# Kernel optimization log

Measured on AMD Instinct MI355X. Metric: run time of the kernel, lower is better.

The kernel has to match this reference:

```python
import jax, jax.numpy as jnp
import numpy as np

B, N, C, F, E, K = 4, 4096, 1024, 4096, 8, 2

def setup_inputs() -> dict:
    key = jax.random.key(0)
    ks = jax.random.split(key, 6)
    x = jax.random.normal(ks[0], (B, N, C), dtype=jnp.float32)
    router_w = jax.random.normal(ks[1], (E, C), dtype=jnp.float32) * 0.02  # nn.Linear weight [out,in]
    w1 = jax.random.normal(ks[2], (E, C, F), dtype=jnp.float32) * (1.0 / np.sqrt(C))
    b1 = jnp.zeros((E, F), dtype=jnp.float32)
    w2 = jax.random.normal(ks[3], (E, F, C), dtype=jnp.float32) * (1.0 / np.sqrt(F))
    b2 = jnp.zeros((E, C), dtype=jnp.float32)
    return {"x": x, "router_w": router_w, "w1": w1, "b1": b1, "w2": w2, "b2": b2}

def reference(x, router_w, w1, b1, w2, b2):
    Bx, Nx, Cx = x.shape
    xf = x.reshape(-1, Cx)                                  # [T, C]
    logits = xf @ router_w.T                                # [T, E]
    probs = jax.nn.softmax(logits, axis=-1)
    top_w, top_i = jax.lax.top_k(probs, K)                  # [T, K]
    top_w = top_w / (jnp.sum(top_w, axis=-1, keepdims=True) + 1e-9)
    out = jnp.zeros_like(xf)
    for e in range(E):
        # combine weight for expert e per token (0 if not routed)
        gate = jnp.sum(jnp.where(top_i == e, top_w, 0.0), axis=-1)   # [T]
        h = jax.nn.gelu(xf @ w1[e] + b1[e], approximate=False)       # [T, F]
        y = h @ w2[e] + b2[e]                                        # [T, C]
        out = out + gate[:, None] * y
    return out.reshape(Bx, Nx, Cx)
```

## Files before the change

### kernel.cpp

```cpp
#include <hip/hip_runtime.h>
#include <hip/hip_fp16.h>

#define T_TOK 16384
#define C_DIM 1024
#define F_DIM 4096
#define E_NUM 8

typedef _Float16 half8 __attribute__((ext_vector_type(8)));
typedef _Float16 half4v __attribute__((ext_vector_type(4)));
typedef float f32x4 __attribute__((ext_vector_type(4)));

static constexpr size_t META_OFF  = 0;
static constexpr size_t XB_OFF    = 256;
static constexpr size_t W1T_OFF   = XB_OFF  + (size_t)2*T_TOK*C_DIM;
static constexpr size_t W2T_OFF   = W1T_OFF + (size_t)2*E_NUM*C_DIM*F_DIM;
static constexpr size_t HB_OFF    = W2T_OFF + (size_t)2*E_NUM*C_DIM*F_DIM;
static constexpr size_t YB_OFF    = HB_OFF  + (size_t)2*T_TOK*2*F_DIM;
static constexpr size_t TOK_OFF   = YB_OFF  + (size_t)2*T_TOK*2*C_DIM;
static constexpr size_t GATE_OFF  = TOK_OFF + (size_t)4*E_NUM*T_TOK;
static constexpr size_t TSLOT_OFF = GATE_OFF+ (size_t)4*E_NUM*T_TOK;
static constexpr size_t EPAIR_OFF = TSLOT_OFF + (size_t)4*T_TOK*2;
static constexpr size_t GPAIR_OFF = EPAIR_OFF + (size_t)4*T_TOK;
static constexpr size_t WS_NEED   = GPAIR_OFF + (size_t)8*T_TOK;

__device__ __forceinline__ void async16(void* lds, const void* g) {
  __builtin_amdgcn_global_load_lds((const __attribute__((address_space(1))) unsigned int*)g,
                                   (__attribute__((address_space(3))) unsigned int*)lds,
                                   16, 0, 0);
}

__global__ __launch_bounds__(256) void transpose_cast_kernel(const float* __restrict__ in,
                                                             _Float16* __restrict__ outp,
                                                             int R, int Cc) {
  __shared__ float tile[64][65];
  int e = blockIdx.z;
  const float* ip = in + (size_t)e * R * Cc;
  _Float16* op = outp + (size_t)e * R * Cc;
  int c0 = blockIdx.x * 64, r0 = blockIdx.y * 64;
  int tid = threadIdx.x;
  int lr = tid >> 4, lc = (tid & 15) * 4;
  #pragma unroll
  for (int d = 0; d < 4; ++d) {
    int row = lr + d * 16;
    float4 v = *(const float4*)(ip + (size_t)(r0 + row) * Cc + c0 + lc);
    tile[row][lc]     = v.x;
    tile[row][lc + 1] = v.y;
    tile[row][lc + 2] = v.z;
    tile[row][lc + 3] = v.w;
  }
  __syncthreads();
  int oc = tid >> 3, or8 = (tid & 7) * 8;
  #pragma unroll
  for (int d = 0; d < 2; ++d) {
    int c = oc + d * 32;
    half8 h;
    #pragma unroll
    for (int j = 0; j < 8; ++j) h[j] = (_Float16)tile[or8 + j][c];
    *(half8*)(op + (size_t)(c0 + c) * R + r0 + or8) = h;
  }
}

__global__ __launch_bounds__(256) void router_kernel(const float* __restrict__ x,
                                                     const float* __restrict__ rw,
                                                     int* __restrict__ epair,
                                                     float2* __restrict__ gpair,
                                                     _Float16* __restrict__ xb) {
  int wv = threadIdx.x >> 6, l = threadIdx.x & 63;
  int t = blockIdx.x * 4 + wv;
  const float* xr = x + (size_t)t * C_DIM;
  double acc[E_NUM] = {};
  #pragma unroll
  for (int j = 0; j < 4; ++j) {
    float4 xv = *(const float4*)(xr + j * 256 + l * 4);
    half4v hv;
    hv[0] = (_Float16)xv.x; hv[1] = (_Float16)xv.y;
    hv[2] = (_Float16)xv.z; hv[3] = (_Float16)xv.w;
    *(half4v*)(xb + (size_t)t * C_DIM + j * 256 + l * 4) = hv;
    #pragma unroll
    for (int e = 0; e < E_NUM; ++e) {
      float4 w4 = *(const float4*)(rw + (size_t)e * C_DIM + j * 256 + l * 4);
      acc[e] += (double)xv.x * w4.x + (double)xv.y * w4.y +
                (double)xv.z * w4.z + (double)xv.w * w4.w;
    }
  }
  #pragma unroll
  for (int e = 0; e < E_NUM; ++e)
    #pragma unroll
    for (int off = 32; off; off >>= 1)
      acc[e] += __shfl_xor(acc[e], off, 64);

  if (l == 0) {
    double m = acc[0];
    #pragma unroll
    for (int e = 1; e < E_NUM; ++e) m = acc[e] > m ? acc[e] : m;
    double p[E_NUM], s = 0.0;
    #pragma unroll
    for (int e = 0; e < E_NUM; ++e) { p[e] = exp(acc[e] - m); s += p[e]; }
    int i0 = 0; double b0 = p[0];
    #pragma unroll
    for (int e = 1; e < E_NUM; ++e) if (p[e] > b0) { b0 = p[e]; i0 = e; }
    int i1 = -1; double b1v = -1.0;
    #pragma unroll
    for (int e = 0; e < E_NUM; ++e) if (e != i0 && p[e] > b1v) { b1v = p[e]; i1 = e; }
    double q0 = b0 / s, q1 = b1v / s;
    double den = q0 + q1 + 1e-9;
    epair[t] = i0 | (i1 << 8);
    gpair[t] = make_float2((float)(q0 / den), (float)(q1 / den));
  }
}

__global__ __launch_bounds__(1024) void assign_kernel(const int* __restrict__ epair,
                                                      const float2* __restrict__ gpair,
                                                      int* __restrict__ counts,
                                                      int* __restrict__ tok,
                                                      float* __restrict__ gate,
                                                      int* __restrict__ tslot) {
  __shared__ int wsum[16];
  __shared__ int wbase[16];
  __shared__ int stot;
  int myE = blockIdx.x;
  int tid = threadIdx.x, wid = tid >> 6, lane = tid & 63;
  int base = 0;
  for (int it = 0; it < (T_TOK * 2) / 1024; ++it) {
    int idx = it * 1024 + tid;
    int t = idx >> 1, k = idx & 1;
    int ep = epair[t];
    int e = (k ? (ep >> 8) : ep) & 0xff;
    bool f = (e == myE);
    unsigned long long mask = __ballot(f);
    int lanep = __popcll(mask & ((1ull << lane) - 1ull));
    if (lane == 0) wsum[wid] = __popcll(mask);
    __syncthreads();
    if (tid == 0) {
      int s = 0;
      #pragma unroll
      for (int i = 0; i < 16; ++i) { wbase[i] = s; s += wsum[i]; }
      stot = s;
    }
    __syncthreads();
    if (f) {
      int slot = base + wbase[wid] + lanep;
      float2 g = gpair[t];
      tok[myE * T_TOK + slot] = t;
      gate[myE * T_TOK + slot] = k ? g.y : g.x;
      tslot[idx] = (myE << 24) | slot;
    }
    base += stot;
  }
  if (tid == 0) counts[myE] = base;
}

__global__ void plan_kernel(int* meta) {
  if (threadIdx.x == 0 && blockIdx.x == 0) {
    int ro = 0, to = 0;
    meta[8] = 0; meta[17] = 0;
    for (int e = 0; e < E_NUM; ++e) {
      int c = meta[e];
      ro += c; to += (c + 127) >> 7;
      meta[9 + e] = ro; meta[18 + e] = to;
    }
  }
}


__global__ __launch_bounds__(512) void gemm1_kernel(const _Float16* __restrict__ xb,
                                                    const _Float16* __restrict__ w1t,
                                                    const float* __restrict__ b1,
                                                    _Float16* __restrict__ hbuf,
                                                    const int* __restrict__ tok,
                                                    const int* __restrict__ meta) {
  __shared__ _Float16 smem[24576];
  __shared__ int tokLds[128];

  int bid = blockIdx.x;
  int swz = (bid & 7) * 528 + (bid >> 3);
  int band = swz >> 7, rem = swz & 127;
  int nt = rem >> 3;
  int mt = band * 8 + (rem & 7);
  if (mt >= meta[17 + E_NUM]) return;
  int e = 0;
  while (mt >= meta[18 + e]) ++e;
  int ne = meta[e];
  int r0 = (mt - meta[17 + e]) << 7;
  int valid = ne - r0; if (valid > 128) valid = 128;

  int tid = threadIdx.x;
  if (tid < 128) {
    int r = tid < valid ? tid : valid - 1;
    tokLds[tid] = tok[e * T_TOK + r0 + r];
  }
  __syncthreads();

  int row = tid >> 2, c4 = tid & 3;
  int ch = c4 ^ ((row >> 1) & 3);
  const _Float16* aSrc  = xb + (size_t)tokLds[row] * C_DIM + ch * 8;
  const _Float16* bSrc0 = w1t + ((size_t)e * F_DIM + nt * 256 + row) * C_DIM + ch * 8;
  const _Float16* bSrc1 = bSrc0 + (size_t)128 * C_DIM;

  char* SM = (char*)smem;
  char* dst = SM + (size_t)tid * 16;

  int w = tid >> 6, l = tid & 63;
  int wm = w >> 2, wn = w & 3;
  int rl = l & 15, q = l >> 4;
  int swq = (q ^ ((rl >> 1) & 3)) * 16;
  int aBy = wm * 4096 + rl * 64 + swq;
  int bBy = 16384 + wn * 4096 + rl * 64 + swq;

  f32x4 acc[4][4] = {};
  constexpr int NT = C_DIM / 64;
  for (int kt = 0; kt < NT; ++kt) {
    __syncthreads();
    int ko = kt * 64;
    async16(dst,          aSrc  + ko);
    async16(dst + 8192,   aSrc  + ko + 32);
    async16(dst + 16384,  bSrc0 + ko);
    async16(dst + 24576,  bSrc1 + ko);
    async16(dst + 32768,  bSrc0 + ko + 32);
    async16(dst + 40960,  bSrc1 + ko + 32);
    __syncthreads();
    #pragma unroll
    for (int ks = 0; ks < 2; ++ks) {
      half8 af[4], bf[4];
      #pragma unroll
      for (int m = 0; m < 4; ++m)
        af[m] = *(const half8*)(SM + ks * 8192 + aBy + m * 1024);
      #pragma unroll
      for (int n = 0; n < 4; ++n)
        bf[n] = *(const half8*)(SM + ks * 16384 + bBy + n * 1024);
      #pragma unroll
      for (int m = 0; m < 4; ++m)
        #pragma unroll
        for (int n = 0; n < 4; ++n)
          acc[m][n] = __builtin_amdgcn_mfma_f32_16x16x32_f16(af[m], bf[n], acc[m][n], 0, 0, 0);
    }
  }

  int hbase = meta[8 + e] + r0;
  float bv[4];
  #pragma unroll
  for (int n = 0; n < 4; ++n)
    bv[n] = b1[(size_t)e * F_DIM + nt * 256 + wn * 64 + n * 16 + rl];
  #pragma unroll
  for (int m = 0; m < 4; ++m) {
    int rb = wm * 64 + m * 16 + q * 4;
    #pragma unroll
    for (int n = 0; n < 4; ++n) {
      int col = nt * 256 + wn * 64 + n * 16 + rl;
      #pragma unroll
      for (int r = 0; r < 4; ++r) {
        int rr = rb + r;
        if (rr < valid) {
          float pre = acc[m][n][r] + bv[n];
          float g = 0.5f * pre * (1.0f + erff(pre * 0.70710678118654752f));
          hbuf[(size_t)(hbase + rr) * F_DIM + col] = (_Float16)g;
        }
      }
    }
  }
}

__global__ __launch_bounds__(256) void gemm2_kernel(const _Float16* __restrict__ hbuf,
                                                    const _Float16* __restrict__ w2t,
                                                    const float* __restrict__ b2,
                                                    _Float16* __restrict__ ybuf,
                                                    const float* __restrict__ gate,
                                                    const int* __restrict__ meta) {
  __shared__ _Float16 smem[16384];
  __shared__ float gateLds[128];

  int bid = blockIdx.x;
  int swz = (bid & 7) * 264 + (bid >> 3);
  int band = swz >> 6, rem = swz & 63;
  int nt = rem >> 3;
  int mt = band * 8 + (rem & 7);
  if (mt >= meta[17 + E_NUM]) return;
  int e = 0;
  while (mt >= meta[18 + e]) ++e;
  int ne = meta[e];
  int r0 = (mt - meta[17 + e]) << 7;
  int valid = ne - r0; if (valid > 128) valid = 128;
  int hbase = meta[8 + e] + r0;

  int tid = threadIdx.x;
  if (tid < 128) {
    int r = tid < valid ? tid : valid - 1;
    gateLds[tid] = gate[e * T_TOK + r0 + r];
  }
  __syncthreads();

  int row = tid >> 2, c4 = tid & 3;
  int ch = c4 ^ ((row >> 1) & 3);
  int rcA0 = row      < valid ? row      : valid - 1;
  int rcA1 = row + 64 < valid ? row + 64 : valid - 1;
  const _Float16* aSrc0 = hbuf + (size_t)(hbase + rcA0) * F_DIM + ch * 8;
  const _Float16* aSrc1 = hbuf + (size_t)(hbase + rcA1) * F_DIM + ch * 8;
  const _Float16* bSrc0 = w2t + ((size_t)e * C_DIM + nt * 128 + row) * F_DIM + ch * 8;
  const _Float16* bSrc1 = bSrc0 + (size_t)64 * F_DIM;

  char* SM = (char*)smem;
  char* dst = SM + (size_t)tid * 16;

  int w = tid >> 6, l = tid & 63;
  int wm = w >> 1, wn = w & 1;
  int rl = l & 15, q = l >> 4;
  int swq = (q ^ ((rl >> 1) & 3)) * 16;
  int aBy = wm * 4096 + rl * 64 + swq;
  int bBy = 16384 + wn * 4096 + rl * 64 + swq;

  f32x4 acc[4][4] = {};
  constexpr int NT = F_DIM / 64;
  for (int kt = 0; kt < NT; ++kt) {
    __syncthreads();
    int ko = kt * 64;
    async16(dst,          aSrc0 + ko);
    async16(dst + 4096,   aSrc1 + ko);
    async16(dst + 8192,   aSrc0 + ko + 32);
    async16(dst + 12288,  aSrc1 + ko + 32);
    async16(dst + 16384,  bSrc0 + ko);
    async16(dst + 20480,  bSrc1 + ko);
    async16(dst + 24576,  bSrc0 + ko + 32);
    async16(dst + 28672,  bSrc1 + ko + 32);
    __syncthreads();
    #pragma unroll
    for (int ks = 0; ks < 2; ++ks) {
      half8 af[4], bf[4];
      #pragma unroll
      for (int m = 0; m < 4; ++m)
        af[m] = *(const half8*)(SM + ks * 8192 + aBy + m * 1024);
      #pragma unroll
      for (int n = 0; n < 4; ++n)
        bf[n] = *(const half8*)(SM + ks * 8192 + bBy + n * 1024);
      #pragma unroll
      for (int m = 0; m < 4; ++m)
        #pragma unroll
        for (int n = 0; n < 4; ++n)
          acc[m][n] = __builtin_amdgcn_mfma_f32_16x16x32_f16(af[m], bf[n], acc[m][n], 0, 0, 0);
    }
  }

  float bv[4];
  #pragma unroll
  for (int n = 0; n < 4; ++n)
    bv[n] = b2[(size_t)e * C_DIM + nt * 128 + wn * 64 + n * 16 + rl];
  #pragma unroll
  for (int m = 0; m < 4; ++m) {
    int rb = wm * 64 + m * 16 + q * 4;
    #pragma unroll
    for (int n = 0; n < 4; ++n) {
      int col = nt * 128 + wn * 64 + n * 16 + rl;
      #pragma unroll
      for (int r = 0; r < 4; ++r) {
        int rr = rb + r;
        if (rr < valid) {
          float val = gateLds[rr] * (acc[m][n][r] + bv[n]);
          ybuf[(size_t)(hbase + rr) * C_DIM + col] = (_Float16)val;
        }
      }
    }
  }
}

__global__ __launch_bounds__(256) void combine_kernel(const _Float16* __restrict__ ybuf,
                                                      const int* __restrict__ tslot,
                                                      const int* __restrict__ meta,
                                                      float* __restrict__ out) {
  int gid = blockIdx.x * 256 + threadIdx.x;
  int t = gid >> 7;
  int cc = (gid & 127) << 3;
  int s0 = tslot[t * 2], s1 = tslot[t * 2 + 1];
  size_t r0 = (size_t)meta[8 + (s0 >> 24)] + (s0 & 0xFFFFFF);
  size_t r1 = (size_t)meta[8 + (s1 >> 24)] + (s1 & 0xFFFFFF);
  half8 y0 = *(const half8*)(ybuf + r0 * C_DIM + cc);
  half8 y1 = *(const half8*)(ybuf + r1 * C_DIM + cc);
  float4 o0, o1;
  o0.x = (float)y0[0] + (float)y1[0];
  o0.y = (float)y0[1] + (float)y1[1];
  o0.z = (float)y0[2] + (float)y1[2];
  o0.w = (float)y0[3] + (float)y1[3];
  o1.x = (float)y0[4] + (float)y1[4];
  o1.y = (float)y0[5] + (float)y1[5];
  o1.z = (float)y0[6] + (float)y1[6];
  o1.w = (float)y0[7] + (float)y1[7];
  *(float4*)(out + (size_t)t * C_DIM + cc) = o0;
  *(float4*)(out + (size_t)t * C_DIM + cc + 4) = o1;
}

extern "C" void kernel_launch(void* const* d_in, const int* in_sizes, int n_in,
                              void* d_out, int out_size, void* d_ws, size_t ws_size,
                              hipStream_t stream) {
  (void)in_sizes; (void)n_in; (void)out_size;
  if (!d_ws || ws_size < WS_NEED) return;

  const float* x  = (const float*)d_in[0];
  const float* rw = (const float*)d_in[1];
  const float* w1 = (const float*)d_in[2];
  const float* b1 = (const float*)d_in[3];
  const float* w2 = (const float*)d_in[4];
  const float* b2 = (const float*)d_in[5];
  float* out = (float*)d_out;

  char* ws = (char*)d_ws;
  int*       meta  = (int*)(ws + META_OFF);
  _Float16*  xb    = (_Float16*)(ws + XB_OFF);
  _Float16*  w1t   = (_Float16*)(ws + W1T_OFF);
  _Float16*  w2t   = (_Float16*)(ws + W2T_OFF);
  _Float16*  hbuf  = (_Float16*)(ws + HB_OFF);
  _Float16*  ybuf  = (_Float16*)(ws + YB_OFF);
  int*       tok   = (int*)(ws + TOK_OFF);
  float*     gate  = (float*)(ws + GATE_OFF);
  int*       tslot = (int*)(ws + TSLOT_OFF);
  int*       epair = (int*)(ws + EPAIR_OFF);
  float2*    gpair = (float2*)(ws + GPAIR_OFF);

  hipMemsetAsync(meta, 0, 256, stream);

  transpose_cast_kernel<<<dim3(F_DIM / 64, C_DIM / 64, E_NUM), 256, 0, stream>>>(w1, w1t, C_DIM, F_DIM);
  transpose_cast_kernel<<<dim3(C_DIM / 64, F_DIM / 64, E_NUM), 256, 0, stream>>>(w2, w2t, F_DIM, C_DIM);
  router_kernel<<<T_TOK / 4, 256, 0, stream>>>(x, rw, epair, gpair, xb);
  assign_kernel<<<E_NUM, 1024, 0, stream>>>(epair, gpair, meta, tok, gate, tslot);
  plan_kernel<<<1, 64, 0, stream>>>(meta);

  gemm1_kernel<<<264 * 16, 512, 0, stream>>>(xb, w1t, b1, hbuf, tok, meta);
  gemm2_kernel<<<264 * 8, 256, 0, stream>>>(hbuf, w2t, b2, ybuf, gate, meta);
  combine_kernel<<<(T_TOK * (C_DIM / 8)) / 256, 256, 0, stream>>>(ybuf, tslot, meta, out);
}
```

Measured before the change: 1.008 ms.

## Make expert GEMMs persistent with grid-stride tile loop and smaller gemm1 tiles

Both expert GEMM kernels become persistent: a fixed grid of 1024 blocks loops over the swizzled work tiles and skips empty ones, instead of launching one block per possible tile and exiting early. gemm1 also shrinks from 512-thread 128x256 tiles to 256-thread 128x128 tiles, matching gemm2. The intent is to cut the cost of launching and retiring many empty blocks and to improve load balance and occupancy. The trade-off is extra per-tile synchronisation, and the smaller gemm1 tile loads the A operand more times per output.

```diff
diff --git a/kernel.cpp b/kernel.cpp
--- a/kernel.cpp
+++ b/kernel.cpp
@@ -163,97 +163,106 @@
 }
 
 
-__global__ __launch_bounds__(512) void gemm1_kernel(const _Float16* __restrict__ xb,
+#define GEMM_GRID 1024
+
+__global__ __launch_bounds__(256) void gemm1_kernel(const _Float16* __restrict__ xb,
                                                     const _Float16* __restrict__ w1t,
                                                     const float* __restrict__ b1,
                                                     _Float16* __restrict__ hbuf,
                                                     const int* __restrict__ tok,
                                                     const int* __restrict__ meta) {
-  __shared__ _Float16 smem[24576];
+  __shared__ _Float16 smem[16384];
   __shared__ int tokLds[128];
 
-  int bid = blockIdx.x;
-  int swz = (bid & 7) * 528 + (bid >> 3);
-  int band = swz >> 7, rem = swz & 127;
-  int nt = rem >> 3;
-  int mt = band * 8 + (rem & 7);
-  if (mt >= meta[17 + E_NUM]) return;
-  int e = 0;
-  while (mt >= meta[18 + e]) ++e;
-  int ne = meta[e];
-  int r0 = (mt - meta[17 + e]) << 7;
-  int valid = ne - r0; if (valid > 128) valid = 128;
-
   int tid = threadIdx.x;
-  if (tid < 128) {
-    int r = tid < valid ? tid : valid - 1;
-    tokLds[tid] = tok[e * T_TOK + r0 + r];
-  }
-  __syncthreads();
-
   int row = tid >> 2, c4 = tid & 3;
   int ch = c4 ^ ((row >> 1) & 3);
-  const _Float16* aSrc  = xb + (size_t)tokLds[row] * C_DIM + ch * 8;
-  const _Float16* bSrc0 = w1t + ((size_t)e * F_DIM + nt * 256 + row) * C_DIM + ch * 8;
-  const _Float16* bSrc1 = bSrc0 + (size_t)128 * C_DIM;
-
-  char* SM = (char*)smem;
-  char* dst = SM + (size_t)tid * 16;
-
-  int w = tid >> 6, l = tid & 63;
-  int wm = w >> 2, wn = w & 3;
+  int w0 = tid >> 6, l = tid & 63;
+  int wm = w0 >> 1, wn = w0 & 1;
   int rl = l & 15, q = l >> 4;
   int swq = (q ^ ((rl >> 1) & 3)) * 16;
   int aBy = wm * 4096 + rl * 64 + swq;
   int bBy = 16384 + wn * 4096 + rl * 64 + swq;
-
-  f32x4 acc[4][4] = {};
-  constexpr int NT = C_DIM / 64;
-  for (int kt = 0; kt < NT; ++kt) {
-    __syncthreads();
-    int ko = kt * 64;
-    async16(dst,          aSrc  + ko);
-    async16(dst + 8192,   aSrc  + ko + 32);
-    async16(dst + 16384,  bSrc0 + ko);
-    async16(dst + 24576,  bSrc1 + ko);
-    async16(dst + 32768,  bSrc0 + ko + 32);
-    async16(dst + 40960,  bSrc1 + ko + 32);
-    __syncthreads();
-    #pragma unroll
-    for (int ks = 0; ks < 2; ++ks) {
-      half8 af[4], bf[4];
+  char* SM = (char*)smem;
+  char* dst = SM + (size_t)tid * 16;
+
+  constexpr int NWORK = 264 * 32;
+  int nTiles = meta[17 + E_NUM];
+
+  for (int wk = blockIdx.x; wk < NWORK; wk += GEMM_GRID) {
+    int swz = (wk & 7) * (NWORK / 8) + (wk >> 3);
+    int band = swz >> 8, rem = swz & 255;
+    int nt = rem >> 3;
+    int mt = band * 8 + (rem & 7);
+    if (mt >= nTiles) continue;
+    int e = 0;
+    while (mt >= meta[18 + e]) ++e;
+    int ne = meta[e];
+    int r0 = (mt - meta[17 + e]) << 7;
+    int valid = ne - r0; if (valid > 128) valid = 128;
+
+    __syncthreads();
+    if (tid < 128) {
+      int r = tid < valid ? tid : valid - 1;
+      tokLds[tid] = tok[e * T_TOK + r0 + r];
+    }
+    __syncthreads();
+
+    const _Float16* aSrc0 = xb + (size_t)tokLds[row] * C_DIM + ch * 8;
+    const _Float16* aSrc1 = xb + (size_t)tokLds[row + 64] * C_DIM + ch * 8;
+    const _Float16* bSrc0 = w1t + ((size_t)e * F_DIM + nt * 128 + row) * C_DIM + ch * 8;
+    const _Float16* bSrc1 = bSrc0 + (size_t)64 * C_DIM;
+
+    f32x4 acc[4][4] = {};
+    constexpr int NT = C_DIM / 64;
+    for (int kt = 0; kt < NT; ++kt) {
+      __syncthreads();
+      int ko = kt * 64;
+      async16(dst,          aSrc0 + ko);
+      async16(dst + 4096,   aSrc1 + ko);
+      async16(dst + 8192,   aSrc0 + ko + 32);
+      async16(dst + 12288,  aSrc1 + ko + 32);
+      async16(dst + 16384,  bSrc0 + ko);
+      async16(dst + 20480,  bSrc1 + ko);
+      async16(dst + 24576,  bSrc0 + ko + 32);
+      async16(dst + 28672,  bSrc1 + ko + 32);
+      __syncthreads();
       #pragma unroll
-      for (int m = 0; m < 4; ++m)
-        af[m] = *(const half8*)(SM + ks * 8192 + aBy + m * 1024);
+      for (int ks = 0; ks < 2; ++ks) {
+        half8 af[4], bf[4];
+        #pragma unroll
+        for (int m = 0; m < 4; ++m)
+          af[m] = *(const half8*)(SM + ks * 8192 + aBy + m * 1024);
+        #pragma unroll
+        for (int n = 0; n < 4; ++n)
+          bf[n] = *(const half8*)(SM + ks * 8192 + bBy + n * 1024);
+        #pragma unroll
+        for (int m = 0; m < 4; ++m)
+          #pragma unroll
+          for (int n = 0; n < 4; ++n)
+            acc[m][n] = __builtin_amdgcn_mfma_f32_16x16x32_f16(af[m], bf[n], acc[m][n], 0, 0, 0);
+      }
+    }
+
+    int hbase = meta[8 + e] + r0;
+    float bv[4];
+    #pragma unroll
+    for (int n = 0; n < 4; ++n)
+      bv[n] = b1[(size_t)e * F_DIM + nt * 128 + wn * 64 + n * 16 + rl];
+    #pragma unroll
+    for (int m = 0; m < 4; ++m) {
+      int rb = wm * 64 + m * 16 + q * 4;
       #pragma unroll
-      for (int n = 0; n < 4; ++n)
-        bf[n] = *(const half8*)(SM + ks * 16384 + bBy + n * 1024);
-      #pragma unroll
-      for (int m = 0; m < 4; ++m)
-        #pragma unroll
-        for (int n = 0; n < 4; ++n)
-          acc[m][n] = __builtin_amdgcn_mfma_f32_16x16x32_f16(af[m], bf[n], acc[m][n], 0, 0, 0);
-    }
-  }
-
-  int hbase = meta[8 + e] + r0;
-  float bv[4];
-  #pragma unroll
-  for (int n = 0; n < 4; ++n)
-    bv[n] = b1[(size_t)e * F_DIM + nt * 256 + wn * 64 + n * 16 + rl];
-  #pragma unroll
-  for (int m = 0; m < 4; ++m) {
-    int rb = wm * 64 + m * 16 + q * 4;
-    #pragma unroll
-    for (int n = 0; n < 4; ++n) {
-      int col = nt * 256 + wn * 64 + n * 16 + rl;
-      #pragma unroll
-      for (int r = 0; r < 4; ++r) {
-        int rr = rb + r;
-        if (rr < valid) {
-          float pre = acc[m][n][r] + bv[n];
-          float g = 0.5f * pre * (1.0f + erff(pre * 0.70710678118654752f));
-          hbuf[(size_t)(hbase + rr) * F_DIM + col] = (_Float16)g;
+      for (int n = 0; n < 4; ++n) {
+        int col = nt * 128 + wn * 64 + n * 16 + rl;
+        #pragma unroll
+        for (int r = 0; r < 4; ++r) {
+          int rr = rb + r;
+          if (rr < valid) {
+            float pre = acc[m][n][r] + bv[n];
+            float g = 0.5f * pre * (1.0f + erff(pre * 0.70710678118654752f));
+            hbuf[(size_t)(hbase + rr) * F_DIM + col] = (_Float16)g;
+          }
         }
       }
     }
@@ -269,92 +278,96 @@
   __shared__ _Float16 smem[16384];
   __shared__ float gateLds[128];
 
-  int bid = blockIdx.x;
-  int swz = (bid & 7) * 264 + (bid >> 3);
-  int band = swz >> 6, rem = swz & 63;
-  int nt = rem >> 3;
-  int mt = band * 8 + (rem & 7);
-  if (mt >= meta[17 + E_NUM]) return;
-  int e = 0;
-  while (mt >= meta[18 + e]) ++e;
-  int ne = meta[e];
-  int r0 = (mt - meta[17 + e]) << 7;
-  int valid = ne - r0; if (valid > 128) valid = 128;
-  int hbase = meta[8 + e] + r0;
-
   int tid = threadIdx.x;
-  if (tid < 128) {
-    int r = tid < valid ? tid : valid - 1;
-    gateLds[tid] = gate[e * T_TOK + r0 + r];
-  }
-  __syncthreads();
-
   int row = tid >> 2, c4 = tid & 3;
   int ch = c4 ^ ((row >> 1) & 3);
-  int rcA0 = row      < valid ? row      : valid - 1;
-  int rcA1 = row + 64 < valid ? row + 64 : valid - 1;
-  const _Float16* aSrc0 = hbuf + (size_t)(hbase + rcA0) * F_DIM + ch * 8;
-  const _Float16* aSrc1 = hbuf + (size_t)(hbase + rcA1) * F_DIM + ch * 8;
-  const _Float16* bSrc0 = w2t + ((size_t)e * C_DIM + nt * 128 + row) * F_DIM + ch * 8;
-  const _Float16* bSrc1 = bSrc0 + (size_t)64 * F_DIM;
-
-  char* SM = (char*)smem;
-  char* dst = SM + (size_t)tid * 16;
-
-  int w = tid >> 6, l = tid & 63;
-  int wm = w >> 1, wn = w & 1;
+  int w0 = tid >> 6, l = tid & 63;
+  int wm = w0 >> 1, wn = w0 & 1;
   int rl = l & 15, q = l >> 4;
   int swq = (q ^ ((rl >> 1) & 3)) * 16;
   int aBy = wm * 4096 + rl * 64 + swq;
   int bBy = 16384 + wn * 4096 + rl * 64 + swq;
-
-  f32x4 acc[4][4] = {};
-  constexpr int NT = F_DIM / 64;
-  for (int kt = 0; kt < NT; ++kt) {
-    __syncthreads();
-    int ko = kt * 64;
-    async16(dst,          aSrc0 + ko);
-    async16(dst + 4096,   aSrc1 + ko);
-    async16(dst + 8192,   aSrc0 + ko + 32);
-    async16(dst + 12288,  aSrc1 + ko + 32);
-    async16(dst + 16384,  bSrc0 + ko);
-    async16(dst + 20480,  bSrc1 + ko);
-    async16(dst + 24576,  bSrc0 + ko + 32);
-    async16(dst + 28672,  bSrc1 + ko + 32);
-    __syncthreads();
-    #pragma unroll
-    for (int ks = 0; ks < 2; ++ks) {
-      half8 af[4], bf[4];
+  char* SM = (char*)smem;
+  char* dst = SM + (size_t)tid * 16;
+
+  constexpr int NWORK = 264 * 8;
+  int nTiles = meta[17 + E_NUM];
+
+  for (int wk = blockIdx.x; wk < NWORK; wk += GEMM_GRID) {
+    int swz = (wk & 7) * (NWORK / 8) + (wk >> 3);
+    int band = swz >> 6, rem = swz & 63;
+    int nt = rem >> 3;
+    int mt = band * 8 + (rem & 7);
+    if (mt >= nTiles) continue;
+    int e = 0;
+    while (mt >= meta[18 + e]) ++e;
+    int ne = meta[e];
+    int r0 = (mt - meta[17 + e]) << 7;
+    int valid = ne - r0; if (valid > 128) valid = 128;
+    int hbase = meta[8 + e] + r0;
+
+    __syncthreads();
+    if (tid < 128) {
+      int r = tid < valid ? tid : valid - 1;
+      gateLds[tid] = gate[e * T_TOK + r0 + r];
+    }
+    __syncthreads();
+
+    int rcA0 = row      < valid ? row      : valid - 1;
+    int rcA1 = row + 64 < valid ? row + 64 : valid - 1;
+    const _Float16* aSrc0 = hbuf + (size_t)(hbase + rcA0) * F_DIM + ch * 8;
+    const _Float16* aSrc1 = hbuf + (size_t)(hbase + rcA1) * F_DIM + ch * 8;
+    const _Float16* bSrc0 = w2t + ((size_t)e * C_DIM + nt * 128 + row) * F_DIM + ch * 8;
+    const _Float16* bSrc1 = bSrc0 + (size_t)64 * F_DIM;
+
+    f32x4 acc[4][4] = {};
+    constexpr int NT = F_DIM / 64;
+    for (int kt = 0; kt < NT; ++kt) {
+      __syncthreads();
+      int ko = kt * 64;
+      async16(dst,          aSrc0 + ko);
+      async16(dst + 4096,   aSrc1 + ko);
+      async16(dst + 8192,   aSrc0 + ko + 32);
+      async16(dst + 12288,  aSrc1 + ko + 32);
+      async16(dst + 16384,  bSrc0 + ko);
+      async16(dst + 20480,  bSrc1 + ko);
+      async16(dst + 24576,  bSrc0 + ko + 32);
+      async16(dst + 28672,  bSrc1 + ko + 32);
+      __syncthreads();
       #pragma unroll
-      for (int m = 0; m < 4; ++m)
-        af[m] = *(const half8*)(SM + ks * 8192 + aBy + m * 1024);
+      for (int ks = 0; ks < 2; ++ks) {
+        half8 af[4], bf[4];
+        #pragma unroll
+        for (int m = 0; m < 4; ++m)
+          af[m] = *(const half8*)(SM + ks * 8192 + aBy + m * 1024);
+        #pragma unroll
+        for (int n = 0; n < 4; ++n)
+          bf[n] = *(const half8*)(SM + ks * 8192 + bBy + n * 1024);
+        #pragma unroll
+        for (int m = 0; m < 4; ++m)
+          #pragma unroll
+          for (int n = 0; n < 4; ++n)
+            acc[m][n] = __builtin_amdgcn_mfma_f32_16x16x32_f16(af[m], bf[n], acc[m][n], 0, 0, 0);
+      }
+    }
+
+    float bv[4];
+    #pragma unroll
+    for (int n = 0; n < 4; ++n)
+      bv[n] = b2[(size_t)e * C_DIM + nt * 128 + wn * 64 + n * 16 + rl];
+    #pragma unroll
+    for (int m = 0; m < 4; ++m) {
+      int rb = wm * 64 + m * 16 + q * 4;
       #pragma unroll
-      for (int n = 0; n < 4; ++n)
-        bf[n] = *(const half8*)(SM + ks * 8192 + bBy + n * 1024);
-      #pragma unroll
-      for (int m = 0; m < 4; ++m)
-        #pragma unroll
-        for (int n = 0; n < 4; ++n)
-          acc[m][n] = __builtin_amdgcn_mfma_f32_16x16x32_f16(af[m], bf[n], acc[m][n], 0, 0, 0);
-    }
-  }
-
-  float bv[4];
-  #pragma unroll
-  for (int n = 0; n < 4; ++n)
-    bv[n] = b2[(size_t)e * C_DIM + nt * 128 + wn * 64 + n * 16 + rl];
-  #pragma unroll
-  for (int m = 0; m < 4; ++m) {
-    int rb = wm * 64 + m * 16 + q * 4;
-    #pragma unroll
-    for (int n = 0; n < 4; ++n) {
-      int col = nt * 128 + wn * 64 + n * 16 + rl;
-      #pragma unroll
-      for (int r = 0; r < 4; ++r) {
-        int rr = rb + r;
-        if (rr < valid) {
-          float val = gateLds[rr] * (acc[m][n][r] + bv[n]);
-          ybuf[(size_t)(hbase + rr) * C_DIM + col] = (_Float16)val;
+      for (int n = 0; n < 4; ++n) {
+        int col = nt * 128 + wn * 64 + n * 16 + rl;
+        #pragma unroll
+        for (int r = 0; r < 4; ++r) {
+          int rr = rb + r;
+          if (rr < valid) {
+            float val = gateLds[rr] * (acc[m][n][r] + bv[n]);
+            ybuf[(size_t)(hbase + rr) * C_DIM + col] = (_Float16)val;
+          }
         }
       }
     }
@@ -421,7 +434,7 @@
   assign_kernel<<<E_NUM, 1024, 0, stream>>>(epair, gpair, meta, tok, gate, tslot);
   plan_kernel<<<1, 64, 0, stream>>>(meta);
 
-  gemm1_kernel<<<264 * 16, 512, 0, stream>>>(xb, w1t, b1, hbuf, tok, meta);
-  gemm2_kernel<<<264 * 8, 256, 0, stream>>>(hbuf, w2t, b2, ybuf, gate, meta);
+  gemm1_kernel<<<GEMM_GRID, 256, 0, stream>>>(xb, w1t, b1, hbuf, tok, meta);
+  gemm2_kernel<<<GEMM_GRID, 256, 0, stream>>>(hbuf, w2t, b2, ybuf, gate, meta);
   combine_kernel<<<(T_TOK * (C_DIM / 8)) / 256, 256, 0, stream>>>(ybuf, tslot, meta, out);
 }
```

Measured after the change: 1.136 ms. +12.7%, slower.
